# Kernel tuning notes

Hardware: AMD Instinct MI355X
Metric: run time of the kernel (lower is better)

## Reference

```python
import jax, jax.numpy as jnp
import numpy as np

N_EMBD = 1024
HEAD_SIZE = 64

def setup_inputs() -> dict:
    key = jax.random.key(0)
    kx, kk, kq, kv = jax.random.split(key, 4)
    B, T = 8, 2048
    x = jax.random.normal(kx, (B, T, N_EMBD), dtype=jnp.float32)
    s = 1.0 / np.sqrt(N_EMBD)  # torch Linear default init scale (kaiming-uniform-ish)
    Wk = jax.random.uniform(kk, (N_EMBD, HEAD_SIZE), jnp.float32, -s, s)
    Wq = jax.random.uniform(kq, (N_EMBD, HEAD_SIZE), jnp.float32, -s, s)
    Wv = jax.random.uniform(kv, (N_EMBD, HEAD_SIZE), jnp.float32, -s, s)
    return {"x": x, "Wk": Wk, "Wq": Wq, "Wv": Wv}

def reference(x, Wk, Wq, Wv):
    # x: (B,T,C); projections to (B,T,H)
    k = jnp.einsum('btc,ch->bth', x, Wk)
    q = jnp.einsum('btc,ch->bth', x, Wq)
    v = jnp.einsum('btc,ch->bth', x, Wv)
    T = x.shape[1]
    scale = k.shape[-1] ** -0.5
    wei = jnp.einsum('bth,bsh->bts', q, k) * scale  # (B,T,T)
    causal = jnp.tril(jnp.ones((T, T), dtype=bool))
    wei = jnp.where(causal, wei, -jnp.inf)
    wei = jax.nn.softmax(wei, axis=-1)
    out = jnp.einsum('bts,bsh->bth', wei, v)  # (B,T,H)
    return out
```

## Files before the change

kernel.cpp:

```cpp
#include <hip/hip_runtime.h>
#include <math.h>

namespace {
constexpr int BATCH = 8;
constexpr int TSEQ  = 2048;
constexpr int CDIM  = 1024;
constexpr int HDIM  = 64;
constexpr int MROWS = BATCH * TSEQ;
constexpr int NTILE = 128;
constexpr int NSLC  = 8;
constexpr float QSCALE = 0.125f * 1.4426950408889634f;
}

typedef __attribute__((ext_vector_type(4))) float  f32x4;
typedef __attribute__((ext_vector_type(8))) short  s16x8;
typedef __attribute__((ext_vector_type(4))) unsigned short u16x4;

__device__ __forceinline__ unsigned short f2bf(float f) {
    union { float f; unsigned u; } c{f};
    unsigned r = c.u + 0x7FFFu + ((c.u >> 16) & 1u);
    return (unsigned short)(r >> 16);
}
__device__ __forceinline__ float bf2f(unsigned short h) {
    union { unsigned u; float f; } c;
    c.u = (unsigned)h << 16;
    return c.f;
}

__global__ __launch_bounds__(256)
void wswz_kernel(const float* __restrict__ Wk, const float* __restrict__ Wq,
                 const float* __restrict__ Wv, unsigned short* __restrict__ swz)
{
    const int idx  = blockIdx.x * 256 + threadIdx.x;
    const int j    = idx & 7;
    const int lane = (idx >> 3) & 63;
    const int rest = idx >> 9;
    const int tn   = rest % 12;
    const int ksg  = rest / 12;
    const int kk   = ksg * 32 + (lane >> 4) * 8 + j;
    const int n    = tn * 16 + (lane & 15);
    float val;
    if (n < 64)       val = Wq[kk * HDIM + n] * QSCALE;
    else if (n < 128) val = Wk[kk * HDIM + (n - 64)];
    else              val = Wv[kk * HDIM + (n - 128)];
    swz[idx] = f2bf(val);
}

__global__ __launch_bounds__(256, 4)
void proj_kernel(const float* __restrict__ x, const unsigned short* __restrict__ swz,
                 unsigned short* __restrict__ q, unsigned short* __restrict__ k,
                 unsigned short* __restrict__ vt)
{
    __shared__ unsigned short xl[16][1032];

    const int tid  = threadIdx.x;
    const int lane = tid & 63, wave = tid >> 6;
    const int quad = lane >> 4, l15 = lane & 15;
    const int cq   = wave;
    const int m0   = blockIdx.x * 16;

    {
        const float* xb = x + (size_t)m0 * CDIM;
        float4 t[16];
        #pragma unroll
        for (int i = 0; i < 16; ++i)
            t[i] = *(const float4*)(xb + i * 1024 + tid * 4);
        #pragma unroll
        for (int i = 0; i < 16; ++i) {
            const int o = i * 1024 + tid * 4;
            u16x4 p;
            p[0] = f2bf(t[i].x); p[1] = f2bf(t[i].y);
            p[2] = f2bf(t[i].z); p[3] = f2bf(t[i].w);
            *(u16x4*)&xl[o >> 10][o & 1023] = p;
        }
    }
    __syncthreads();

    f32x4 acc[3] = {};
    const unsigned short* bp = swz + ((size_t)(cq * 3) * 64 + lane) * 8;
    s16x8 b0 = *(const s16x8*)(bp);
    s16x8 b1 = *(const s16x8*)(bp + 512);
    s16x8 b2 = *(const s16x8*)(bp + 1024);
    bp += 6144;

    #pragma unroll
    for (int ks = 0; ks < 32; ++ks) {
        s16x8 nb0, nb1, nb2;
        if (ks < 31) {
            nb0 = *(const s16x8*)(bp);
            nb1 = *(const s16x8*)(bp + 512);
            nb2 = *(const s16x8*)(bp + 1024);
            bp += 6144;
        }
        const s16x8 af = *(const s16x8*)&xl[l15][ks * 32 + quad * 8];
        acc[0] = __builtin_amdgcn_mfma_f32_16x16x32_bf16(af, b0, acc[0], 0, 0, 0);
        acc[1] = __builtin_amdgcn_mfma_f32_16x16x32_bf16(af, b1, acc[1], 0, 0, 0);
        acc[2] = __builtin_amdgcn_mfma_f32_16x16x32_bf16(af, b2, acc[2], 0, 0, 0);
        if (ks < 31) { b0 = nb0; b1 = nb1; b2 = nb2; }
    }

    const int rowg = m0 + quad * 4;
    #pragma unroll
    for (int t = 0; t < 3; ++t) {
        const int n = cq * 48 + t * 16 + l15;
        if (n < 64) {
            #pragma unroll
            for (int r = 0; r < 4; ++r)
                q[(size_t)(rowg + r) * HDIM + n] = f2bf(acc[t][r]);
        } else if (n < 128) {
            #pragma unroll
            for (int r = 0; r < 4; ++r)
                k[(size_t)(rowg + r) * HDIM + (n - 64)] = f2bf(acc[t][r]);
        } else {
            const int h  = n - 128;
            const int bb = rowg >> 11, tl = rowg & 2047;
            u16x4 pv;
            #pragma unroll
            for (int r = 0; r < 4; ++r) pv[r] = f2bf(acc[t][r]);
            *(u16x4*)(vt + ((size_t)bb * HDIM + h) * TSEQ + tl) = pv;
        }
    }
}

__global__ __launch_bounds__(256, 4)
void attn_part(const unsigned short* __restrict__ q, const unsigned short* __restrict__ k,
               const unsigned short* __restrict__ vt, unsigned short* __restrict__ Opart,
               float* __restrict__ lpart)
{
    __shared__ unsigned short Kb[4096];
    __shared__ unsigned short Vb[4096];
    __shared__ unsigned short Pl[4][16][72];

    const int tid  = threadIdx.x;
    const int lane = tid & 63, wave = tid >> 6;
    const int quad = lane >> 4, l15 = lane & 15;
    const int b    = blockIdx.y;
    const int p    = blockIdx.x >> 3;
    const int s    = blockIdx.x & 7;

    const unsigned short* qb  = q  + (size_t)b * TSEQ * HDIM;
    const unsigned short* kb  = k  + (size_t)b * TSEQ * HDIM;
    const unsigned short* vtb = vt + (size_t)b * HDIM * TSEQ;

    const int rs = tid >> 3, cgs = tid & 7;
    const int d0 = (((cgs >> 2) * 4 + (rs >> 4)) * 64 + (cgs & 3) * 16 + (rs & 15)) * 8;
    const int rs2 = rs + 32;
    const int d1 = (((cgs >> 2) * 4 + (rs2 >> 4)) * 64 + (cgs & 3) * 16 + (rs2 & 15)) * 8;

    for (int tsel = 0; tsel < 2; ++tsel) {
        const int t   = (tsel == 0) ? p : 31 - p;
        const int m0w = t * 64 + wave * 16;
        const int nt  = t + 1;

        const s16x8 aq0 = *(const s16x8*)(qb + (size_t)(m0w + l15) * HDIM + quad * 8);
        const s16x8 aq1 = *(const s16x8*)(qb + (size_t)(m0w + l15) * HDIM + 32 + quad * 8);

        f32x4 O[4] = {};
        float l_lane[4] = {0.f, 0.f, 0.f, 0.f};

        if (s < nt) {
            {
                const int n0 = s * 64;
                const s16x8 ka = *(const s16x8*)(kb + (size_t)(n0 + rs) * HDIM + cgs * 8);
                const s16x8 kc = *(const s16x8*)(kb + (size_t)(n0 + rs2) * HDIM + cgs * 8);
                const s16x8 va = *(const s16x8*)(vtb + (size_t)rs * TSEQ + n0 + cgs * 8);
                const s16x8 vc = *(const s16x8*)(vtb + (size_t)rs2 * TSEQ + n0 + cgs * 8);
                *(s16x8*)&Kb[d0] = ka; *(s16x8*)&Kb[d1] = kc;
                *(s16x8*)&Vb[d0] = va; *(s16x8*)&Vb[d1] = vc;
            }
            __syncthreads();

            for (int c = s; c < nt; c += 8) {
                const bool pref = (c + 8) < nt;
                s16x8 ka, kc, va, vc;
                if (pref) {
                    const int n0n = (c + 8) * 64;
                    ka = *(const s16x8*)(kb + (size_t)(n0n + rs) * HDIM + cgs * 8);
                    kc = *(const s16x8*)(kb + (size_t)(n0n + rs2) * HDIM + cgs * 8);
                    va = *(const s16x8*)(vtb + (size_t)rs * TSEQ + n0n + cgs * 8);
                    vc = *(const s16x8*)(vtb + (size_t)rs2 * TSEQ + n0n + cgs * 8);
                }

                f32x4 S[4] = {};
                #pragma unroll
                for (int st = 0; st < 4; ++st) {
                    const s16x8 k0 = *(const s16x8*)&Kb[(st * 64 + lane) * 8];
                    const s16x8 k1 = *(const s16x8*)&Kb[((4 + st) * 64 + lane) * 8];
                    S[st] = __builtin_amdgcn_mfma_f32_16x16x32_bf16(aq0, k0, S[st], 0, 0, 0);
                    S[st] = __builtin_amdgcn_mfma_f32_16x16x32_bf16(aq1, k1, S[st], 0, 0, 0);
                }
                __syncthreads();
                if (pref) { *(s16x8*)&Kb[d0] = ka; *(s16x8*)&Kb[d1] = kc; }

                const int n0 = c * 64;
                if (c == t) {
                    const int rowbase = m0w + quad * 4;
                    #pragma unroll
                    for (int st = 0; st < 4; ++st) {
                        const int col = n0 + st * 16 + l15;
                        #pragma unroll
                        for (int r = 0; r < 4; ++r) {
                            const float pv = (col > rowbase + r) ? 0.f : exp2f(S[st][r]);
                            S[st][r] = pv;
                            l_lane[r] += pv;
                        }
                    }
                } else {
                    #pragma unroll
                    for (int st = 0; st < 4; ++st)
                        #pragma unroll
                        for (int r = 0; r < 4; ++r) {
                            const float pv = exp2f(S[st][r]);
                            S[st][r] = pv;
                            l_lane[r] += pv;
                        }
                }

                #pragma unroll
                for (int st = 0; st < 4; ++st)
                    #pragma unroll
                    for (int r = 0; r < 4; ++r)
                        Pl[wave][quad * 4 + r][st * 16 + l15] = f2bf(S[st][r]);
                const s16x8 pa0 = *(const s16x8*)&Pl[wave][l15][quad * 8];
                const s16x8 pa1 = *(const s16x8*)&Pl[wave][l15][32 + quad * 8];

                #pragma unroll
                for (int hst = 0; hst < 4; ++hst) {
                    const s16x8 v0 = *(const s16x8*)&Vb[(hst * 64 + lane) * 8];
                    const s16x8 v1 = *(const s16x8*)&Vb[((4 + hst) * 64 + lane) * 8];
                    O[hst] = __builtin_amdgcn_mfma_f32_16x16x32_bf16(pa0, v0, O[hst], 0, 0, 0);
                    O[hst] = __builtin_amdgcn_mfma_f32_16x16x32_bf16(pa1, v1, O[hst], 0, 0, 0);
                }
                __syncthreads();
                if (pref) { *(s16x8*)&Vb[d0] = va; *(s16x8*)&Vb[d1] = vc; }
            }
            __syncthreads();
        }

        #pragma unroll
        for (int off = 1; off < 16; off <<= 1)
            #pragma unroll
            for (int r = 0; r < 4; ++r)
                l_lane[r] += __shfl_xor(l_lane[r], off);

        const int ti16 = t * 4 + wave;
        const size_t pi = ((size_t)b * NTILE + ti16) * NSLC + s;
        #pragma unroll
        for (int hst = 0; hst < 4; ++hst)
            #pragma unroll
            for (int r = 0; r < 4; ++r)
                Opart[(pi * 16 + quad * 4 + r) * HDIM + hst * 16 + l15] = f2bf(O[hst][r]);
        if (l15 == 0) {
            #pragma unroll
            for (int r = 0; r < 4; ++r)
                lpart[pi * 16 + quad * 4 + r] = l_lane[r];
        }
    }
}

__global__ __launch_bounds__(256)
void attn_combine(const unsigned short* __restrict__ Opart, const float* __restrict__ lpart,
                  float* __restrict__ out)
{
    const int g   = blockIdx.x * 256 + threadIdx.x;
    const int row = g >> 4;
    const int c4  = (g & 15) << 2;
    const int b   = row >> 11, t = row & 2047;
    const int ti  = t >> 4,  r = t & 15;
    const size_t p0 = ((size_t)b * NTILE + ti) * NSLC;

    float acc[4] = {0.f, 0.f, 0.f, 0.f};
    float lv = 0.f;
    #pragma unroll
    for (int s = 0; s < NSLC; ++s) {
        const u16x4 t4 = *(const u16x4*)(Opart + ((p0 + s) * 16 + r) * HDIM + c4);
        #pragma unroll
        for (int j = 0; j < 4; ++j) acc[j] += bf2f(t4[j]);
        lv += lpart[(p0 + s) * 16 + r];
    }
    const float inv = 1.f / lv;
    float4 o = {acc[0] * inv, acc[1] * inv, acc[2] * inv, acc[3] * inv};
    *(float4*)(out + (size_t)row * HDIM + c4) = o;
}

extern "C" void kernel_launch(void* const* d_in, const int* in_sizes, int n_in,
                              void* d_out, int out_size, void* d_ws, size_t ws_size,
                              hipStream_t stream) {
    const float* x  = (const float*)d_in[0];
    const float* Wk = (const float*)d_in[1];
    const float* Wq = (const float*)d_in[2];
    const float* Wv = (const float*)d_in[3];
    float* out = (float*)d_out;

    unsigned short* swz = (unsigned short*)d_ws;
    unsigned short* qw  = swz + 196608;
    unsigned short* kw  = qw + (size_t)MROWS * HDIM;
    unsigned short* vtw = kw + (size_t)MROWS * HDIM;
    unsigned short* Opart = vtw + (size_t)MROWS * HDIM;
    float* lpart = (float*)(Opart + (size_t)BATCH * NTILE * NSLC * 16 * HDIM);

    wswz_kernel<<<dim3(768), 256, 0, stream>>>(Wk, Wq, Wv, swz);
    proj_kernel<<<dim3(MROWS / 16), 256, 0, stream>>>(x, swz, qw, kw, vtw);
    attn_part<<<dim3(16 * NSLC, BATCH), 256, 0, stream>>>(qw, kw, vtw, Opart, lpart);
    attn_combine<<<dim3(MROWS * 16 / 256), 256, 0, stream>>>(Opart, lpart, out);
}
```

Before: 136.0 us.

## Fuse split-KV combine into attention kernel via last-arriver atomic counter

Removes the separate combine kernel. Each attention block now increments a per-(batch, tile) atomic counter after writing its partial O and l, and the eighth block to arrive reduces all slices and writes the final output. A hipMemsetAsync is added to reset the counters, and one __syncthreads at the end of the KV-tile loop is dropped. This saves one kernel launch and one pass over Opart from a separate kernel, at the cost of thread fences, atomics and an unbalanced tail in the last-arriving blocks.

```diff
diff --git a/kernel.cpp b/kernel.cpp
--- a/kernel.cpp
+++ b/kernel.cpp
@@ -125,11 +125,13 @@
 __global__ __launch_bounds__(256, 4)
 void attn_part(const unsigned short* __restrict__ q, const unsigned short* __restrict__ k,
                const unsigned short* __restrict__ vt, unsigned short* __restrict__ Opart,
-               float* __restrict__ lpart)
+               float* __restrict__ lpart, int* __restrict__ cnt,
+               float* __restrict__ out)
 {
     __shared__ unsigned short Kb[4096];
     __shared__ unsigned short Vb[4096];
     __shared__ unsigned short Pl[4][16][72];
+    __shared__ int arrv;
 
     const int tid  = threadIdx.x;
     const int lane = tid & 63, wave = tid >> 6;
@@ -234,7 +236,6 @@
                 __syncthreads();
                 if (pref) { *(s16x8*)&Vb[d0] = va; *(s16x8*)&Vb[d1] = vc; }
             }
-            __syncthreads();
         }
 
         #pragma unroll
@@ -255,32 +256,39 @@
             for (int r = 0; r < 4; ++r)
                 lpart[pi * 16 + quad * 4 + r] = l_lane[r];
         }
+
+        __threadfence();
+        __syncthreads();
+        if (tid == 0) arrv = atomicAdd(&cnt[b * 32 + t], 1);
+        __syncthreads();
+        if (arrv == 7) {
+            __threadfence();
+            const int r  = tid >> 2;
+            const int cg = (tid & 3) << 4;
+            const int tI = t * 4 + (r >> 4);
+            const int rr = r & 15;
+            const size_t pb = ((size_t)b * NTILE + tI) * NSLC;
+            float lv = 0.f;
+            #pragma unroll
+            for (int s2 = 0; s2 < NSLC; ++s2) lv += lpart[(pb + s2) * 16 + rr];
+            const float inv = 1.f / lv;
+            float* orow = out + ((size_t)b * TSEQ + t * 64 + r) * HDIM;
+            #pragma unroll
+            for (int j = 0; j < 4; ++j) {
+                const int c4 = cg + j * 4;
+                float a0 = 0.f, a1 = 0.f, a2 = 0.f, a3 = 0.f;
+                #pragma unroll
+                for (int s2 = 0; s2 < NSLC; ++s2) {
+                    const u16x4 t4 = *(const u16x4*)(Opart + ((pb + s2) * 16 + rr) * HDIM + c4);
+                    a0 += bf2f(t4[0]); a1 += bf2f(t4[1]);
+                    a2 += bf2f(t4[2]); a3 += bf2f(t4[3]);
+                }
+                float4 o = {a0 * inv, a1 * inv, a2 * inv, a3 * inv};
+                *(float4*)(orow + c4) = o;
+            }
+        }
+        __syncthreads();
     }
-}
-
-__global__ __launch_bounds__(256)
-void attn_combine(const unsigned short* __restrict__ Opart, const float* __restrict__ lpart,
-                  float* __restrict__ out)
-{
-    const int g   = blockIdx.x * 256 + threadIdx.x;
-    const int row = g >> 4;
-    const int c4  = (g & 15) << 2;
-    const int b   = row >> 11, t = row & 2047;
-    const int ti  = t >> 4,  r = t & 15;
-    const size_t p0 = ((size_t)b * NTILE + ti) * NSLC;
-
-    float acc[4] = {0.f, 0.f, 0.f, 0.f};
-    float lv = 0.f;
-    #pragma unroll
-    for (int s = 0; s < NSLC; ++s) {
-        const u16x4 t4 = *(const u16x4*)(Opart + ((p0 + s) * 16 + r) * HDIM + c4);
-        #pragma unroll
-        for (int j = 0; j < 4; ++j) acc[j] += bf2f(t4[j]);
-        lv += lpart[(p0 + s) * 16 + r];
-    }
-    const float inv = 1.f / lv;
-    float4 o = {acc[0] * inv, acc[1] * inv, acc[2] * inv, acc[3] * inv};
-    *(float4*)(out + (size_t)row * HDIM + c4) = o;
 }
 
 extern "C" void kernel_launch(void* const* d_in, const int* in_sizes, int n_in,
@@ -298,9 +306,10 @@
     unsigned short* vtw = kw + (size_t)MROWS * HDIM;
     unsigned short* Opart = vtw + (size_t)MROWS * HDIM;
     float* lpart = (float*)(Opart + (size_t)BATCH * NTILE * NSLC * 16 * HDIM);
-
+    int*   cnt   = (int*)(lpart + (size_t)BATCH * NTILE * NSLC * 16);
+
+    hipMemsetAsync(cnt, 0, BATCH * 32 * sizeof(int), stream);
     wswz_kernel<<<dim3(768), 256, 0, stream>>>(Wk, Wq, Wv, swz);
     proj_kernel<<<dim3(MROWS / 16), 256, 0, stream>>>(x, swz, qw, kw, vtw);
-    attn_part<<<dim3(16 * NSLC, BATCH), 256, 0, stream>>>(qw, kw, vtw, Opart, lpart);
-    attn_combine<<<dim3(MROWS * 16 / 256), 256, 0, stream>>>(Opart, lpart, out);
-}
+    attn_part<<<dim3(16 * NSLC, BATCH), 256, 0, stream>>>(qw, kw, vtw, Opart, lpart, cnt, out);
+}
```

Result: slower. 453.9 us (+233.6%).
